# Kernel optimization log

Hardware: AMD Instinct MI355X
Metric: run time of the kernel (lower is better)

The kernel has to match this reference:

```python
import jax, jax.numpy as jnp
import numpy as np

N_HEAD = 16

def setup_inputs() -> dict:
    key = jax.random.key(0)
    k1, k2, k3 = jax.random.split(key, 3)
    B, T, D = 1, 2048, 1024
    x = jax.random.normal(k1, (B, T, D), dtype=jnp.float32)
    # torch Linear(d, 3d, bias=False): y = x @ W.T with W [3d, d]; store transposed [d, 3d]
    W_qkv = jax.random.normal(k2, (D, 3 * D), dtype=jnp.float32) * 0.02
    W_o = jax.random.normal(k3, (D, D), dtype=jnp.float32) * 0.02
    return {"x": x, "W_qkv": W_qkv, "W_o": W_o}

def reference(x, W_qkv, W_o):
    B, T, D = x.shape
    H = N_HEAD
    hd = D // H
    qkv = (x @ W_qkv).reshape(B, T, 3, H, hd)
    q, k, v = qkv[:, :, 0], qkv[:, :, 1], qkv[:, :, 2]  # [B, T, H, hd]
    scale = 1.0 / np.sqrt(hd).astype(np.float32)
    # The per-chunk loop with growing context + mask is exactly dense causal attention.
    att = jnp.einsum('bqhd,bkhd->bhqk', q, k) * scale  # [B, H, T, T]
    causal = jnp.tril(jnp.ones((T, T), dtype=bool))
    att = jnp.where(causal[None, None], att, jnp.finfo(att.dtype).min)
    att = jax.nn.softmax(att, axis=-1)
    y = jnp.einsum('bhqk,bkhd->bqhd', att, v).reshape(B, T, D)
    return y @ W_o
```

## Files before the change

kernel.cpp:

```cpp
#include <hip/hip_runtime.h>
#include <hip/hip_bf16.h>


using u16 = unsigned short;
typedef __attribute__((ext_vector_type(8))) __bf16 bf16x8;
typedef __attribute__((ext_vector_type(8))) unsigned short u16x8;
typedef __attribute__((ext_vector_type(4))) float f32x4;

__device__ __forceinline__ u16 f2bf(float f) {
  union { float f; unsigned u; } v; v.f = f;
  unsigned r = v.u + 0x7FFFu + ((v.u >> 16) & 1u);
  return (u16)(r >> 16);
}

__device__ __forceinline__ float bf2f(u16 b) {
  union { unsigned u; float f; } v; v.u = ((unsigned)b) << 16;
  return v.f;
}

__device__ __forceinline__ unsigned cvt_pk_bf16(float lo, float hi) {
  unsigned r;
  asm("v_cvt_pk_bf16_f32 %0, %1, %2" : "=v"(r) : "v"(lo), "v"(hi));
  return r;
}

__device__ __forceinline__ void gload_lds16(const void* g, void* l) {
  __builtin_amdgcn_global_load_lds((const __attribute__((address_space(1))) void*)g,
                                   (__attribute__((address_space(3))) void*)l, 16, 0, 0);
}

__device__ __forceinline__ f32x4 mfma16(bf16x8 a, bf16x8 b, f32x4 c) {
  return __builtin_amdgcn_mfma_f32_16x16x32_bf16(a, b, c, 0, 0, 0);
}

__global__ __launch_bounds__(256) void cvt_bf16_kernel(const float* __restrict__ in,
                                                       u16* __restrict__ out, int n) {
  int i = (blockIdx.x * 256 + threadIdx.x) * 8;
  if (i >= n) return;
  float4 a = *(const float4*)(in + i);
  float4 b = *(const float4*)(in + i + 4);
  u16x8 r;
  r[0] = f2bf(a.x); r[1] = f2bf(a.y); r[2] = f2bf(a.z); r[3] = f2bf(a.w);
  r[4] = f2bf(b.x); r[5] = f2bf(b.y); r[6] = f2bf(b.z); r[7] = f2bf(b.w);
  *(u16x8*)(out + i) = r;
}

__global__ __launch_bounds__(256) void transpose_bf16_kernel(const float* __restrict__ in,
                                                             u16* __restrict__ out,
                                                             int R, int C) {
  __shared__ u16 tile[32][33];
  const int c0 = blockIdx.x * 32, r0 = blockIdx.y * 32;
  const int tx = threadIdx.x & 31, ty = threadIdx.x >> 5;
#pragma unroll
  for (int rr = ty; rr < 32; rr += 8)
    tile[rr][tx] = f2bf(in[(size_t)(r0 + rr) * C + (c0 + tx)]);
  __syncthreads();
#pragma unroll
  for (int rr = ty; rr < 32; rr += 8)
    out[(size_t)(c0 + rr) * R + (r0 + tx)] = tile[tx][rr];
}

template <typename OutT>
__global__ __launch_bounds__(256) void gemm_bt_kernel(const u16* __restrict__ A,
                                                      const u16* __restrict__ Bt,
                                                      OutT* __restrict__ C,
                                                      int M, int N, int K) {
  constexpr int BM = 128, BN = 128, BK = 32;
  __shared__ u16 As[2][BM * BK];
  __shared__ u16 Bs[2][BN * BK];
  const int tid = threadIdx.x;
  const int lane = tid & 63, wid = tid >> 6;
  const int l16 = lane & 15, l4 = lane >> 4;
  const int wr = (wid >> 1) * 64, wc = (wid & 1) * 64;
  const long bm = (long)blockIdx.x * BM, bn = (long)blockIdx.y * BN;

  f32x4 acc[4][4] = {};
  const int KT = K / BK;

  auto stage = [&](int buf, int kt) {
    const int k0 = kt * BK;
#pragma unroll
    for (int half = 0; half < 2; ++half) {
      int t = half * 256 + tid;
      int row = t >> 2, c8 = (t & 3) << 3;
      gload_lds16(A + (bm + row) * (size_t)K + k0 + c8, &As[buf][row * BK + c8]);
    }
#pragma unroll
    for (int half = 0; half < 2; ++half) {
      int t = half * 256 + tid;
      int row = t >> 2, c8 = (t & 3) << 3;
      gload_lds16(Bt + (bn + row) * (size_t)K + k0 + c8, &Bs[buf][row * BK + c8]);
    }
  };

  stage(0, 0);
  __syncthreads();
  int cur = 0;
  for (int kt = 0; kt < KT; ++kt) {
    if (kt + 1 < KT) stage(cur ^ 1, kt + 1);
    bf16x8 af[4], bfr[4];
#pragma unroll
    for (int m = 0; m < 4; ++m)
      af[m] = *(const bf16x8*)&As[cur][(wr + m * 16 + l16) * BK + l4 * 8];
#pragma unroll
    for (int n = 0; n < 4; ++n)
      bfr[n] = *(const bf16x8*)&Bs[cur][(wc + n * 16 + l16) * BK + l4 * 8];
#pragma unroll
    for (int m = 0; m < 4; ++m)
#pragma unroll
      for (int n = 0; n < 4; ++n)
        acc[m][n] = mfma16(af[m], bfr[n], acc[m][n]);
    __syncthreads();
    cur ^= 1;
  }

#pragma unroll
  for (int m = 0; m < 4; ++m) {
    const long row0 = bm + wr + m * 16 + l4 * 4;
#pragma unroll
    for (int n = 0; n < 4; ++n) {
      const long col = bn + wc + n * 16 + l16;
#pragma unroll
      for (int j = 0; j < 4; ++j) {
        float v = acc[m][n][j];
        if constexpr (sizeof(OutT) == 2)
          C[(row0 + j) * N + col] = (OutT)f2bf(v);
        else
          C[(row0 + j) * N + col] = (OutT)v;
      }
    }
  }
}

__global__ __launch_bounds__(256, 4) void attn_kernel(const u16* __restrict__ qkv,
                                                      u16* __restrict__ opart,
                                                      float2* __restrict__ ml, int S) {
  constexpr int W = 3072;
  const int p = blockIdx.x, h = blockIdx.y, s = blockIdx.z;
  const int tid = threadIdx.x, wid = tid >> 6, lane = tid & 63;
  const int l16 = lane & 15, l4 = lane >> 4;
  const int w0 = (33 * s) / S, w1 = (33 * (s + 1)) / S;

  __shared__ u16 Ks[2][64 * 64];
  __shared__ u16 Vt[2][64][72];

  constexpr float cl2 = 0.125f * 1.44269504f;
  const int vpos = (lane & 32) | ((lane & 12) << 1) | ((lane & 16) >> 2) | (lane & 3);

  auto stageK = [&](int buf, int k0) {
#pragma unroll
    for (int half = 0; half < 2; ++half) {
      int t = half * 256 + tid;
      int row = t >> 3, chunk = t & 7;
      int srcChunk = chunk ^ (row & 7);
      gload_lds16(qkv + (size_t)(k0 + row) * W + 1024 + h * 64 + srcChunk * 8,
                  &Ks[buf][t * 8]);
    }
  };

  bool didA = false, didB = false;
  int w = w0;
  while (w < w1) {
    const bool isA = (w <= p);
    const int qt = isA ? p : 31 - p;
    const int wend = isA ? ((w1 < p + 1) ? w1 : (p + 1)) : w1;
    const int kvb = isA ? 0 : p + 1;
    if (isA) didA = true; else didB = true;

    const int q0 = qt * 64;
    const int qr = q0 + wid * 16 + l16;

    const u16* qrow = qkv + (size_t)(q0 + wid * 16 + l16) * W + h * 64;
    const bf16x8 qa0 = *(const bf16x8*)(qrow + l4 * 8);
    const bf16x8 qa1 = *(const bf16x8*)(qrow + 32 + l4 * 8);

    f32x4 o[4] = {};
    float mrow = -3e38f, lrow = 0.f;

    {
      const int k0 = (w - kvb) * 64;
      stageK(0, k0);
      const u16* vsrc = qkv + (size_t)(k0 + lane) * W + 2048 + h * 64 + wid * 16;
      u16x8 a = *(const u16x8*)vsrc;
      u16x8 b = *(const u16x8*)(vsrc + 8);
#pragma unroll
      for (int i = 0; i < 8; ++i) Vt[0][wid * 16 + i][vpos] = a[i];
#pragma unroll
      for (int i = 0; i < 8; ++i) Vt[0][wid * 16 + 8 + i][vpos] = b[i];
      __syncthreads();
    }

    int cur = 0;
    for (; w < wend; ++w) {
      const int kv = w - kvb;
      const int k0 = kv * 64;
      const bool pf = (w + 1 < wend);

      u16x8 va, vb2;
      if (pf) {
        stageK(cur ^ 1, k0 + 64);
        const u16* vsrc = qkv + (size_t)(k0 + 64 + lane) * W + 2048 + h * 64 + wid * 16;
        va = *(const u16x8*)vsrc;
        vb2 = *(const u16x8*)(vsrc + 8);
      }

      f32x4 sv[4];
#pragma unroll
      for (int nb = 0; nb < 4; ++nb) {
        const int krow = nb * 16 + l16;
        const char* kbase = (const char*)&Ks[cur][0] + krow * 128;
        const int swz = (krow & 7) << 4;
        bf16x8 kb0 = *(const bf16x8*)(kbase + ((l4 * 16) ^ swz));
        bf16x8 kb1 = *(const bf16x8*)(kbase + ((64 + l4 * 16) ^ swz));
        f32x4 z = {0.f, 0.f, 0.f, 0.f};
        z = mfma16(kb0, qa0, z);
        sv[nb] = mfma16(kb1, qa1, z);
      }

      float pv[4][4];
      const bool diag = (kv == qt);
#pragma unroll
      for (int nb = 0; nb < 4; ++nb)
#pragma unroll
        for (int j = 0; j < 4; ++j) {
          float v = sv[nb][j] * cl2;
          if (diag) {
            const int key = k0 + nb * 16 + l4 * 4 + j;
            v = (key <= qr) ? v : -3e38f;
          }
          pv[nb][j] = v;
        }

      float rmax = -3e38f;
#pragma unroll
      for (int nb = 0; nb < 4; ++nb)
#pragma unroll
        for (int j = 0; j < 4; ++j) rmax = fmaxf(rmax, pv[nb][j]);
      rmax = fmaxf(rmax, __shfl_xor(rmax, 16));
      rmax = fmaxf(rmax, __shfl_xor(rmax, 32));

      const float mnew = fmaxf(mrow, rmax);
      if (__any(mnew > mrow)) {
        const float sc = exp2f(mrow - mnew);
        mrow = mnew;
        lrow *= sc;
#pragma unroll
        for (int db = 0; db < 4; ++db)
#pragma unroll
          for (int j = 0; j < 4; ++j) o[db][j] *= sc;
      }

      float rsum = 0.f;
#pragma unroll
      for (int nb = 0; nb < 4; ++nb)
#pragma unroll
        for (int j = 0; j < 4; ++j) {
          const float e = exp2f(pv[nb][j] - mrow);
          pv[nb][j] = e;
          rsum += e;
        }
      rsum += __shfl_xor(rsum, 16);
      rsum += __shfl_xor(rsum, 32);
      lrow += rsum;

      uint4 pk0, pk1;
      pk0.x = cvt_pk_bf16(pv[0][0], pv[0][1]);
      pk0.y = cvt_pk_bf16(pv[0][2], pv[0][3]);
      pk0.z = cvt_pk_bf16(pv[1][0], pv[1][1]);
      pk0.w = cvt_pk_bf16(pv[1][2], pv[1][3]);
      pk1.x = cvt_pk_bf16(pv[2][0], pv[2][1]);
      pk1.y = cvt_pk_bf16(pv[2][2], pv[2][3]);
      pk1.z = cvt_pk_bf16(pv[3][0], pv[3][1]);
      pk1.w = cvt_pk_bf16(pv[3][2], pv[3][3]);

#pragma unroll
      for (int db = 0; db < 4; ++db) {
        bf16x8 va0 = *(const bf16x8*)&Vt[cur][db * 16 + l16][l4 * 8];
        bf16x8 va1 = *(const bf16x8*)&Vt[cur][db * 16 + l16][32 + l4 * 8];
        o[db] = mfma16(va0, *(const bf16x8*)&pk0, o[db]);
        o[db] = mfma16(va1, *(const bf16x8*)&pk1, o[db]);
      }

      if (pf) {
#pragma unroll
        for (int i = 0; i < 8; ++i) Vt[cur ^ 1][wid * 16 + i][vpos] = va[i];
#pragma unroll
        for (int i = 0; i < 8; ++i) Vt[cur ^ 1][wid * 16 + 8 + i][vpos] = vb2[i];
      }
      __syncthreads();
      cur ^= 1;
    }

    {
      const size_t q = q0 + wid * 16 + l16;
      u16* orow = opart + ((q * 16 + h) * S + s) * 64;
#pragma unroll
      for (int db = 0; db < 4; ++db) {
        uint2 w2;
        w2.x = cvt_pk_bf16(o[db][0], o[db][1]);
        w2.y = cvt_pk_bf16(o[db][2], o[db][3]);
        *(uint2*)&orow[db * 16 + l4 * 4] = w2;
      }
      if (l4 == 0)
        ml[(q * 16 + h) * S + s] = make_float2(mrow, lrow);
    }
  }

  if (!didA && tid < 64)
    ml[((size_t)(p * 64 + tid) * 16 + h) * S + s] = make_float2(-3e38f, 0.f);
  if (!didB && tid < 64)
    ml[((size_t)((31 - p) * 64 + tid) * 16 + h) * S + s] = make_float2(-3e38f, 0.f);
}

__global__ __launch_bounds__(256) void combine_kernel(const u16* __restrict__ opart,
                                                      const float2* __restrict__ ml,
                                                      u16* __restrict__ y, int S) {
  const int p = blockIdx.x * 4 + (threadIdx.x >> 6);
  const int d = threadIdx.x & 63;
  float M = -3e38f;
  for (int s = 0; s < S; ++s) M = fmaxf(M, ml[(size_t)p * S + s].x);
  float num = 0.f, den = 0.f;
  for (int s = 0; s < S; ++s) {
    const float2 m2 = ml[(size_t)p * S + s];
    const float w = exp2f(m2.x - M);
    num += w * bf2f(opart[((size_t)p * S + s) * 64 + d]);
    den += w * m2.y;
  }
  const int q = p >> 4, h = p & 15;
  y[(size_t)q * 1024 + h * 64 + d] = f2bf(num / den);
}

extern "C" void kernel_launch(void* const* d_in, const int* in_sizes, int n_in,
                              void* d_out, int out_size, void* d_ws, size_t ws_size,
                              hipStream_t stream) {
  constexpr int T = 2048, D = 1024;
  const float* x    = (const float*)d_in[0];
  const float* Wqkv = (const float*)d_in[1];
  const float* Wo   = (const float*)d_in[2];
  float* out = (float*)d_out;

  u16* xb    = (u16*)d_ws;
  u16* WqkvT = xb + (size_t)T * D;
  u16* WoT   = WqkvT + (size_t)3 * D * D;
  u16* qkv   = WoT + (size_t)D * D;
  u16* yb    = qkv + (size_t)T * 3 * D;

  const size_t baseB = (size_t)(T * D + 3 * D * D + D * D + T * 3 * D + T * D) * 2;
  auto needB = [&](int S) {
    return baseB + (size_t)T * 16 * S * 64 * 2 + (size_t)T * 16 * S * 8;
  };
  const int S = (ws_size >= needB(4)) ? 4 : 2;
  u16*    opart = (u16*)((char*)d_ws + baseB);
  float2* ml    = (float2*)((char*)d_ws + baseB + (size_t)T * 16 * S * 64 * 2);

  cvt_bf16_kernel<<<(T * D) / (256 * 8), 256, 0, stream>>>(x, xb, T * D);
  transpose_bf16_kernel<<<dim3(3 * D / 32, D / 32), 256, 0, stream>>>(Wqkv, WqkvT, D, 3 * D);
  transpose_bf16_kernel<<<dim3(D / 32, D / 32), 256, 0, stream>>>(Wo, WoT, D, D);

  gemm_bt_kernel<u16><<<dim3(T / 128, 3 * D / 128), 256, 0, stream>>>(xb, WqkvT, qkv, T, 3 * D, D);

  attn_kernel<<<dim3(16, 16, S), 256, 0, stream>>>(qkv, opart, ml, S);
  combine_kernel<<<T * 16 / 4, 256, 0, stream>>>(opart, ml, yb, S);

  gemm_bt_kernel<float><<<dim3(T / 128, D / 128), 256, 0, stream>>>(yb, WoT, out, T, D, D);
}
```

Baseline: 111.0 us.

## Fuse prep kernels, swizzle V tile, defer rescale, raise split count and occupancy

Merges the x conversion and two weight transposes into one launch, which removes two kernel launch overheads. In attention, the padded V LDS tile becomes an unpadded XOR-swizzled layout, which saves LDS and lets occupancy rise to 5 blocks per CU. The online-softmax rescale is skipped unless the max grows by more than 8 (lazy rescaling). The row-sum shuffle reduction moves out of the loop, and s_setprio is raised around the MFMA sections. KV splits go from 4 to 5 when the workspace allows it, which adds more partials for the combine step to merge.

```diff
diff --git a/kernel.cpp b/kernel.cpp
--- a/kernel.cpp
+++ b/kernel.cpp
@@ -33,23 +33,33 @@
   return __builtin_amdgcn_mfma_f32_16x16x32_bf16(a, b, c, 0, 0, 0);
 }
 
-__global__ __launch_bounds__(256) void cvt_bf16_kernel(const float* __restrict__ in,
-                                                       u16* __restrict__ out, int n) {
-  int i = (blockIdx.x * 256 + threadIdx.x) * 8;
-  if (i >= n) return;
-  float4 a = *(const float4*)(in + i);
-  float4 b = *(const float4*)(in + i + 4);
-  u16x8 r;
-  r[0] = f2bf(a.x); r[1] = f2bf(a.y); r[2] = f2bf(a.z); r[3] = f2bf(a.w);
-  r[4] = f2bf(b.x); r[5] = f2bf(b.y); r[6] = f2bf(b.z); r[7] = f2bf(b.w);
-  *(u16x8*)(out + i) = r;
-}
-
-__global__ __launch_bounds__(256) void transpose_bf16_kernel(const float* __restrict__ in,
-                                                             u16* __restrict__ out,
-                                                             int R, int C) {
+__global__ __launch_bounds__(256) void prep_kernel(const float* __restrict__ x,
+                                                   const float* __restrict__ Wqkv,
+                                                   const float* __restrict__ Wo,
+                                                   u16* __restrict__ xb,
+                                                   u16* __restrict__ WqkvT,
+                                                   u16* __restrict__ WoT) {
   __shared__ u16 tile[32][33];
-  const int c0 = blockIdx.x * 32, r0 = blockIdx.y * 32;
+  const int b = blockIdx.x;
+  if (b < 1024) {
+    const int i = (b * 256 + threadIdx.x) * 8;
+    float4 a = *(const float4*)(x + i);
+    float4 c = *(const float4*)(x + i + 4);
+    u16x8 r;
+    r[0] = f2bf(a.x); r[1] = f2bf(a.y); r[2] = f2bf(a.z); r[3] = f2bf(a.w);
+    r[4] = f2bf(c.x); r[5] = f2bf(c.y); r[6] = f2bf(c.z); r[7] = f2bf(c.w);
+    *(u16x8*)(xb + i) = r;
+    return;
+  }
+  const float* in; u16* out; int R, C, bx, by;
+  if (b < 1024 + 3072) {
+    const int tb = b - 1024;
+    in = Wqkv; out = WqkvT; R = 1024; C = 3072; bx = tb % 96; by = tb / 96;
+  } else {
+    const int tb = b - 4096;
+    in = Wo; out = WoT; R = 1024; C = 1024; bx = tb % 32; by = tb / 32;
+  }
+  const int c0 = bx * 32, r0 = by * 32;
   const int tx = threadIdx.x & 31, ty = threadIdx.x >> 5;
 #pragma unroll
   for (int rr = ty; rr < 32; rr += 8)
@@ -132,7 +142,7 @@
   }
 }
 
-__global__ __launch_bounds__(256, 4) void attn_kernel(const u16* __restrict__ qkv,
+__global__ __launch_bounds__(256, 5) void attn_kernel(const u16* __restrict__ qkv,
                                                       u16* __restrict__ opart,
                                                       float2* __restrict__ ml, int S) {
   constexpr int W = 3072;
@@ -142,7 +152,7 @@
   const int w0 = (33 * s) / S, w1 = (33 * (s + 1)) / S;
 
   __shared__ u16 Ks[2][64 * 64];
-  __shared__ u16 Vt[2][64][72];
+  __shared__ u16 Vt[2][64][64];
 
   constexpr float cl2 = 0.125f * 1.44269504f;
   const int vpos = (lane & 32) | ((lane & 12) << 1) | ((lane & 16) >> 2) | (lane & 3);
@@ -175,7 +185,7 @@
     const bf16x8 qa1 = *(const bf16x8*)(qrow + 32 + l4 * 8);
 
     f32x4 o[4] = {};
-    float mrow = -3e38f, lrow = 0.f;
+    float mrow = -3e38f, lsum = 0.f;
 
     {
       const int k0 = (w - kvb) * 64;
@@ -184,9 +194,11 @@
       u16x8 a = *(const u16x8*)vsrc;
       u16x8 b = *(const u16x8*)(vsrc + 8);
 #pragma unroll
-      for (int i = 0; i < 8; ++i) Vt[0][wid * 16 + i][vpos] = a[i];
-#pragma unroll
-      for (int i = 0; i < 8; ++i) Vt[0][wid * 16 + 8 + i][vpos] = b[i];
+      for (int i = 0; i < 8; ++i)
+        Vt[0][wid * 16 + i][vpos ^ ((i & 7) << 3)] = a[i];
+#pragma unroll
+      for (int i = 0; i < 8; ++i)
+        Vt[0][wid * 16 + 8 + i][vpos ^ ((i & 7) << 3)] = b[i];
       __syncthreads();
     }
 
@@ -205,6 +217,7 @@
       }
 
       f32x4 sv[4];
+      __builtin_amdgcn_s_setprio(1);
 #pragma unroll
       for (int nb = 0; nb < 4; ++nb) {
         const int krow = nb * 16 + l16;
@@ -216,6 +229,7 @@
         z = mfma16(kb0, qa0, z);
         sv[nb] = mfma16(kb1, qa1, z);
       }
+      __builtin_amdgcn_s_setprio(0);
 
       float pv[4][4];
       const bool diag = (kv == qt);
@@ -240,28 +254,24 @@
       rmax = fmaxf(rmax, __shfl_xor(rmax, 32));
 
       const float mnew = fmaxf(mrow, rmax);
-      if (__any(mnew > mrow)) {
+      if (__any(mnew - mrow > 8.f)) {
         const float sc = exp2f(mrow - mnew);
         mrow = mnew;
-        lrow *= sc;
+        lsum *= sc;
 #pragma unroll
         for (int db = 0; db < 4; ++db)
 #pragma unroll
           for (int j = 0; j < 4; ++j) o[db][j] *= sc;
       }
 
-      float rsum = 0.f;
 #pragma unroll
       for (int nb = 0; nb < 4; ++nb)
 #pragma unroll
         for (int j = 0; j < 4; ++j) {
           const float e = exp2f(pv[nb][j] - mrow);
           pv[nb][j] = e;
-          rsum += e;
+          lsum += e;
         }
-      rsum += __shfl_xor(rsum, 16);
-      rsum += __shfl_xor(rsum, 32);
-      lrow += rsum;
 
       uint4 pk0, pk1;
       pk0.x = cvt_pk_bf16(pv[0][0], pv[0][1]);
@@ -273,24 +283,32 @@
       pk1.z = cvt_pk_bf16(pv[3][0], pv[3][1]);
       pk1.w = cvt_pk_bf16(pv[3][2], pv[3][3]);
 
+      const int swzv = (l16 & 7) << 3;
+      __builtin_amdgcn_s_setprio(1);
 #pragma unroll
       for (int db = 0; db < 4; ++db) {
-        bf16x8 va0 = *(const bf16x8*)&Vt[cur][db * 16 + l16][l4 * 8];
-        bf16x8 va1 = *(const bf16x8*)&Vt[cur][db * 16 + l16][32 + l4 * 8];
+        bf16x8 va0 = *(const bf16x8*)&Vt[cur][db * 16 + l16][(l4 * 8) ^ swzv];
+        bf16x8 va1 = *(const bf16x8*)&Vt[cur][db * 16 + l16][(32 + l4 * 8) ^ swzv];
         o[db] = mfma16(va0, *(const bf16x8*)&pk0, o[db]);
         o[db] = mfma16(va1, *(const bf16x8*)&pk1, o[db]);
       }
+      __builtin_amdgcn_s_setprio(0);
 
       if (pf) {
 #pragma unroll
-        for (int i = 0; i < 8; ++i) Vt[cur ^ 1][wid * 16 + i][vpos] = va[i];
-#pragma unroll
-        for (int i = 0; i < 8; ++i) Vt[cur ^ 1][wid * 16 + 8 + i][vpos] = vb2[i];
+        for (int i = 0; i < 8; ++i)
+          Vt[cur ^ 1][wid * 16 + i][vpos ^ ((i & 7) << 3)] = va[i];
+#pragma unroll
+        for (int i = 0; i < 8; ++i)
+          Vt[cur ^ 1][wid * 16 + 8 + i][vpos ^ ((i & 7) << 3)] = vb2[i];
       }
       __syncthreads();
       cur ^= 1;
     }
 
+    float lrow = lsum;
+    lrow += __shfl_xor(lrow, 16);
+    lrow += __shfl_xor(lrow, 32);
     {
       const size_t q = q0 + wid * 16 + l16;
       u16* orow = opart + ((q * 16 + h) * S + s) * 64;
@@ -304,6 +322,7 @@
       if (l4 == 0)
         ml[(q * 16 + h) * S + s] = make_float2(mrow, lrow);
     }
+    lsum = 0.f;
   }
 
   if (!didA && tid < 64)
@@ -349,13 +368,11 @@
   auto needB = [&](int S) {
     return baseB + (size_t)T * 16 * S * 64 * 2 + (size_t)T * 16 * S * 8;
   };
-  const int S = (ws_size >= needB(4)) ? 4 : 2;
+  const int S = (ws_size >= needB(5)) ? 5 : ((ws_size >= needB(4)) ? 4 : 2);
   u16*    opart = (u16*)((char*)d_ws + baseB);
   float2* ml    = (float2*)((char*)d_ws + baseB + (size_t)T * 16 * S * 64 * 2);
 
-  cvt_bf16_kernel<<<(T * D) / (256 * 8), 256, 0, stream>>>(x, xb, T * D);
-  transpose_bf16_kernel<<<dim3(3 * D / 32, D / 32), 256, 0, stream>>>(Wqkv, WqkvT, D, 3 * D);
-  transpose_bf16_kernel<<<dim3(D / 32, D / 32), 256, 0, stream>>>(Wo, WoT, D, D);
+  prep_kernel<<<1024 + 3072 + 1024, 256, 0, stream>>>(x, Wqkv, Wo, xb, WqkvT, WoT);
 
   gemm_bt_kernel<u16><<<dim3(T / 128, 3 * D / 128), 256, 0, stream>>>(xb, WqkvT, qkv, T, 3 * D, D);
 
```

Result: slower. 121.3 us (+9.2%).
